# Kernel optimization log

Measured on AMD Instinct MI355X. Metric: run time of the kernel, lower is better.

The kernel has to match this reference:

```python
import jax, jax.numpy as jnp
import numpy as np

N = 8192      # grid points along the differentiated axis (axis=0)
B = 4096      # trailing batch/feature dim
S = 7         # stencil width (order=2, acc=4)


def _make_offsets(n, s):
    # Interior stencil is centered (-3..3); near boundaries the stencil is
    # shifted one-sided so that i + off stays in [0, n-1], matching the
    # precomputed one-sided boundary stencils of a non-uniform FD operator.
    i = np.arange(n)[:, None]                      # [n, 1]
    base = np.arange(s)[None, :] - s // 2          # [1, s]
    idx = np.clip(i + base, 0, n - 1)
    # de-duplicate clipped indices by re-spreading near boundaries
    lo_shift = np.maximum(0, (s // 2) - np.arange(n))[:, None]
    hi_shift = np.maximum(0, (s // 2) - (n - 1 - np.arange(n)))[:, None]
    idx = i + base + lo_shift - hi_shift           # valid, distinct indices
    return (idx - i).astype(np.int32)              # offsets relative to i


def setup_inputs() -> dict:
    key = jax.random.key(0)
    k1, k2 = jax.random.split(key)
    y = jax.random.normal(k1, (N, B), dtype=jnp.float32)
    all_coefficients = jax.random.normal(k2, (N, S), dtype=jnp.float32)
    all_offsets = jnp.asarray(_make_offsets(N, S))  # int32 [N, S]
    return {"y": y, "all_coefficients": all_coefficients, "all_offsets": all_offsets}


def reference(y, all_coefficients, all_offsets):
    # axis = 0, so y is already in 'moved' layout y_m.
    # Original: for each i, yd[i] = sum_s ws[i,s] * y[i + offs[i,s]]
    # (sequential fori_loop). Vectorized over all grid points i:
    n = y.shape[0]
    idxs = jnp.arange(n, dtype=all_offsets.dtype)[:, None] + all_offsets  # [n, S]
    stencil = jnp.take(y, idxs, axis=0)              # [n, S, B] gather
    yd = jnp.einsum('ns,ns...->n...', all_coefficients, stencil)
    return yd
```

## Files before the change

kernel.cpp:

```cpp
#include <hip/hip_runtime.h>


#define FD_N   8192
#define FD_B   4096
#define FD_S   7
#define FD_R   2
#define HALO   3
#define WIN    (FD_R + 2 * HALO)
#define NSTRIP (FD_N / FD_R)
#define NCHUNK 4
#define NWG    (NSTRIP * NCHUNK)
#define NXCD   8

typedef float v4f __attribute__((ext_vector_type(4)));

__global__ __launch_bounds__(256) void
_FinDiffNonUniform_51608327029442_kernel(const float* __restrict__ y,
                                         const float* __restrict__ coef,
                                         const int*   __restrict__ offs,
                                         float*       __restrict__ out) {
    const int bid   = blockIdx.x;
    const int id    = (bid & (NXCD - 1)) * (NWG / NXCD) + (bid >> 3);
    const int strip = id & (NSTRIP - 1);
    const int chunk = id >> 12;
    const int n0    = strip * FD_R;
    const int b     = (chunk << 10) + (threadIdx.x << 2);

    if (strip >= 2 && strip <= NSTRIP - 3) {
        float c[FD_R][FD_S];
#pragma unroll
        for (int r = 0; r < FD_R; ++r)
#pragma unroll
            for (int s = 0; s < FD_S; ++s)
                c[r][s] = coef[(size_t)(n0 + r) * FD_S + s];

        const float* ybase = y + (size_t)(n0 - HALO) * FD_B + b;

        v4f w[WIN];
#pragma unroll
        for (int j = 0; j < WIN; ++j)
            w[j] = *reinterpret_cast<const v4f*>(ybase + (size_t)j * FD_B);

        asm volatile("" ::: "memory");

        v4f acc[FD_R];
#pragma unroll
        for (int r = 0; r < FD_R; ++r)
            acc[r] = (v4f){0.f, 0.f, 0.f, 0.f};

#pragma unroll
        for (int j = 0; j < WIN; ++j) {
#pragma unroll
            for (int r = 0; r < FD_R; ++r) {
                const int s = j - r;
                if (s >= 0 && s < FD_S)
                    acc[r] += c[r][s] * w[j];
            }
        }

#pragma unroll
        for (int r = 0; r < FD_R; ++r)
            __builtin_nontemporal_store(
                acc[r], reinterpret_cast<v4f*>(out + (size_t)(n0 + r) * FD_B + b));
    } else {
#pragma unroll
        for (int r = 0; r < FD_R; ++r) {
            const int n = n0 + r;
            v4f acc = (v4f){0.f, 0.f, 0.f, 0.f};
#pragma unroll
            for (int s = 0; s < FD_S; ++s) {
                const float cc = coef[(size_t)n * FD_S + s];
                const int   o  = offs[(size_t)n * FD_S + s];
                const v4f   v  =
                    *reinterpret_cast<const v4f*>(y + (size_t)(n + o) * FD_B + b);
                acc += cc * v;
            }
            __builtin_nontemporal_store(
                acc, reinterpret_cast<v4f*>(out + (size_t)n * FD_B + b));
        }
    }
}

extern "C" void kernel_launch(void* const* d_in, const int* in_sizes, int n_in,
                              void* d_out, int out_size, void* d_ws, size_t ws_size,
                              hipStream_t stream) {
    const float* y    = (const float*)d_in[0];
    const float* coef = (const float*)d_in[1];
    const int*   offs = (const int*)d_in[2];
    float*       out  = (float*)d_out;

    _FinDiffNonUniform_51608327029442_kernel<<<NWG, 256, 0, stream>>>(y, coef, offs, out);
}
```

Measured before the change: 232.3 us.

## Stream a sliding register window over 32-row spans with prefetched rows

```diff
diff --git a/kernel.cpp b/kernel.cpp
--- a/kernel.cpp
+++ b/kernel.cpp
@@ -4,12 +4,14 @@
 #define FD_N   8192
 #define FD_B   4096
 #define FD_S   7
-#define FD_R   2
 #define HALO   3
-#define WIN    (FD_R + 2 * HALO)
-#define NSTRIP (FD_N / FD_R)
+#define STEP   4
+#define WIN    (STEP + 2 * HALO)
+#define SPAN   32
+#define NITER  (SPAN / STEP)
+#define NSPAN  (FD_N / SPAN)
 #define NCHUNK 4
-#define NWG    (NSTRIP * NCHUNK)
+#define NWG    (NSPAN * NCHUNK)
 #define NXCD   8
 
 typedef float v4f __attribute__((ext_vector_type(4)));
@@ -21,50 +23,14 @@
                                          float*       __restrict__ out) {
     const int bid   = blockIdx.x;
     const int id    = (bid & (NXCD - 1)) * (NWG / NXCD) + (bid >> 3);
-    const int strip = id & (NSTRIP - 1);
-    const int chunk = id >> 12;
-    const int n0    = strip * FD_R;
+    const int span  = id & (NSPAN - 1);
+    const int chunk = id >> 8;
+    const int n0    = span * SPAN;
     const int b     = (chunk << 10) + (threadIdx.x << 2);
 
-    if (strip >= 2 && strip <= NSTRIP - 3) {
-        float c[FD_R][FD_S];
-#pragma unroll
-        for (int r = 0; r < FD_R; ++r)
-#pragma unroll
-            for (int s = 0; s < FD_S; ++s)
-                c[r][s] = coef[(size_t)(n0 + r) * FD_S + s];
-
-        const float* ybase = y + (size_t)(n0 - HALO) * FD_B + b;
-
-        v4f w[WIN];
-#pragma unroll
-        for (int j = 0; j < WIN; ++j)
-            w[j] = *reinterpret_cast<const v4f*>(ybase + (size_t)j * FD_B);
-
-        asm volatile("" ::: "memory");
-
-        v4f acc[FD_R];
-#pragma unroll
-        for (int r = 0; r < FD_R; ++r)
-            acc[r] = (v4f){0.f, 0.f, 0.f, 0.f};
-
-#pragma unroll
-        for (int j = 0; j < WIN; ++j) {
-#pragma unroll
-            for (int r = 0; r < FD_R; ++r) {
-                const int s = j - r;
-                if (s >= 0 && s < FD_S)
-                    acc[r] += c[r][s] * w[j];
-            }
-        }
-
-#pragma unroll
-        for (int r = 0; r < FD_R; ++r)
-            __builtin_nontemporal_store(
-                acc[r], reinterpret_cast<v4f*>(out + (size_t)(n0 + r) * FD_B + b));
-    } else {
-#pragma unroll
-        for (int r = 0; r < FD_R; ++r) {
+    if (span == 0 || span == NSPAN - 1) {
+#pragma unroll 4
+        for (int r = 0; r < SPAN; ++r) {
             const int n = n0 + r;
             v4f acc = (v4f){0.f, 0.f, 0.f, 0.f};
 #pragma unroll
@@ -77,6 +43,54 @@
             }
             __builtin_nontemporal_store(
                 acc, reinterpret_cast<v4f*>(out + (size_t)n * FD_B + b));
+        }
+        return;
+    }
+
+    const float* ybase = y   + (size_t)(n0 - HALO) * FD_B + b;
+    float*       obase = out + (size_t)n0          * FD_B + b;
+
+    v4f w[WIN];
+#pragma unroll
+    for (int j = 0; j < WIN; ++j)
+        w[j] = *reinterpret_cast<const v4f*>(ybase + (size_t)j * FD_B);
+    asm volatile("" ::: "memory");
+
+#pragma unroll
+    for (int k = 0; k < NITER; ++k) {
+        const int a = k * STEP;
+
+        v4f p[STEP];
+        if (k + 1 < NITER) {
+#pragma unroll
+            for (int j = 0; j < STEP; ++j)
+                p[j] = *reinterpret_cast<const v4f*>(
+                           ybase + (size_t)(a + WIN + j) * FD_B);
+            asm volatile("" ::: "memory");
+        }
+
+        float c[STEP][FD_S];
+#pragma unroll
+        for (int r = 0; r < STEP; ++r)
+#pragma unroll
+            for (int s = 0; s < FD_S; ++s)
+                c[r][s] = coef[(size_t)(n0 + a + r) * FD_S + s];
+
+#pragma unroll
+        for (int r = 0; r < STEP; ++r) {
+            v4f acc = c[r][0] * w[r];
+#pragma unroll
+            for (int s = 1; s < FD_S; ++s)
+                acc += c[r][s] * w[r + s];
+            __builtin_nontemporal_store(
+                acc, reinterpret_cast<v4f*>(obase + (size_t)(a + r) * FD_B));
+        }
+
+        if (k + 1 < NITER) {
+#pragma unroll
+            for (int j = 0; j < WIN - STEP; ++j) w[j] = w[j + STEP];
+#pragma unroll
+            for (int j = 0; j < STEP; ++j)       w[WIN - STEP + j] = p[j];
         }
     }
 }
```

Measured after the change: 258.3 us. 11.2% more time.

## Stage stencil window in LDS via global_load_lds with larger row strips

Applied to the files above, without the earlier changes.

```diff
diff --git a/kernel.cpp b/kernel.cpp
--- a/kernel.cpp
+++ b/kernel.cpp
@@ -4,81 +4,96 @@
 #define FD_N   8192
 #define FD_B   4096
 #define FD_S   7
-#define FD_R   2
+#define FD_R   8
 #define HALO   3
 #define WIN    (FD_R + 2 * HALO)
 #define NSTRIP (FD_N / FD_R)
-#define NCHUNK 4
+#define CHUNKF 1024
+#define NCHUNK (FD_B / CHUNKF)
 #define NWG    (NSTRIP * NCHUNK)
-#define NXCD   8
 
 typedef float v4f __attribute__((ext_vector_type(4)));
+typedef unsigned int u32;
 
 __global__ __launch_bounds__(256) void
 _FinDiffNonUniform_51608327029442_kernel(const float* __restrict__ y,
                                          const float* __restrict__ coef,
                                          const int*   __restrict__ offs,
                                          float*       __restrict__ out) {
-    const int bid   = blockIdx.x;
-    const int id    = (bid & (NXCD - 1)) * (NWG / NXCD) + (bid >> 3);
-    const int strip = id & (NSTRIP - 1);
-    const int chunk = id >> 12;
+    const int strip = blockIdx.x >> 2;
+    const int chunk = blockIdx.x & 3;
     const int n0    = strip * FD_R;
-    const int b     = (chunk << 10) + (threadIdx.x << 2);
+    const int tid   = threadIdx.x;
+    const int b     = (chunk << 10) + (tid << 2);
 
-    if (strip >= 2 && strip <= NSTRIP - 3) {
-        float c[FD_R][FD_S];
-#pragma unroll
-        for (int r = 0; r < FD_R; ++r)
-#pragma unroll
-            for (int s = 0; s < FD_S; ++s)
-                c[r][s] = coef[(size_t)(n0 + r) * FD_S + s];
+    __shared__ float lds[WIN * CHUNKF];
 
-        const float* ybase = y + (size_t)(n0 - HALO) * FD_B + b;
-
-        v4f w[WIN];
-#pragma unroll
-        for (int j = 0; j < WIN; ++j)
-            w[j] = *reinterpret_cast<const v4f*>(ybase + (size_t)j * FD_B);
-
-        asm volatile("" ::: "memory");
-
-        v4f acc[FD_R];
-#pragma unroll
-        for (int r = 0; r < FD_R; ++r)
-            acc[r] = (v4f){0.f, 0.f, 0.f, 0.f};
-
-#pragma unroll
-        for (int j = 0; j < WIN; ++j) {
-#pragma unroll
-            for (int r = 0; r < FD_R; ++r) {
-                const int s = j - r;
-                if (s >= 0 && s < FD_S)
-                    acc[r] += c[r][s] * w[j];
-            }
-        }
-
-#pragma unroll
-        for (int r = 0; r < FD_R; ++r)
-            __builtin_nontemporal_store(
-                acc[r], reinterpret_cast<v4f*>(out + (size_t)(n0 + r) * FD_B + b));
-    } else {
+    if (strip == 0 || strip == NSTRIP - 1) {
 #pragma unroll
         for (int r = 0; r < FD_R; ++r) {
             const int n = n0 + r;
+            const float* __restrict__ c = coef + (size_t)n * FD_S;
+            const int*   __restrict__ o = offs + (size_t)n * FD_S;
             v4f acc = (v4f){0.f, 0.f, 0.f, 0.f};
 #pragma unroll
             for (int s = 0; s < FD_S; ++s) {
-                const float cc = coef[(size_t)n * FD_S + s];
-                const int   o  = offs[(size_t)n * FD_S + s];
-                const v4f   v  =
-                    *reinterpret_cast<const v4f*>(y + (size_t)(n + o) * FD_B + b);
-                acc += cc * v;
+                const v4f v = *reinterpret_cast<const v4f*>(
+                    y + (size_t)(n + o[s]) * FD_B + b);
+                acc += c[s] * v;
             }
             __builtin_nontemporal_store(
                 acc, reinterpret_cast<v4f*>(out + (size_t)n * FD_B + b));
         }
+        return;
     }
+
+    const int base = n0 - HALO;
+    const int wave = tid >> 6;
+    const int lane = tid & 63;
+
+    const char* gsrc = (const char*)y
+                     + (size_t)base * (FD_B * 4)
+                     + (size_t)chunk * (CHUNKF * 4)
+                     + (size_t)wave * 1024
+                     + (size_t)lane * 16;
+    u32* lbase = reinterpret_cast<u32*>(lds) + wave * 256;
+
+#pragma unroll
+    for (int j = 0; j < WIN; ++j) {
+        __builtin_amdgcn_global_load_lds(
+            (const __attribute__((address_space(1))) u32*)(gsrc + (size_t)j * (FD_B * 4)),
+            (__attribute__((address_space(3))) u32*)(lbase + j * CHUNKF),
+            16, 0, 0);
+    }
+    __syncthreads();
+
+    float c[FD_R][FD_S];
+#pragma unroll
+    for (int r = 0; r < FD_R; ++r)
+#pragma unroll
+        for (int s = 0; s < FD_S; ++s)
+            c[r][s] = coef[(size_t)(n0 + r) * FD_S + s];
+
+    v4f acc[FD_R];
+#pragma unroll
+    for (int r = 0; r < FD_R; ++r)
+        acc[r] = (v4f){0.f, 0.f, 0.f, 0.f};
+
+#pragma unroll
+    for (int j = 0; j < WIN; ++j) {
+        const v4f v = *reinterpret_cast<const v4f*>(&lds[j * CHUNKF + tid * 4]);
+#pragma unroll
+        for (int r = 0; r < FD_R; ++r) {
+            const int s = j - r;
+            if (s >= 0 && s < FD_S)
+                acc[r] += c[r][s] * v;
+        }
+    }
+
+#pragma unroll
+    for (int r = 0; r < FD_R; ++r)
+        __builtin_nontemporal_store(
+            acc[r], reinterpret_cast<v4f*>(out + (size_t)(n0 + r) * FD_B + b));
 }
 
 extern "C" void kernel_launch(void* const* d_in, const int* in_sizes, int n_in,
```

Measured after the change: 230.9 us. About the same (-0.6%).

## Stream rows through an LDS ring buffer with async global-to-LDS loads

Applied to the files above, without the earlier changes.

```diff
diff --git a/kernel.cpp b/kernel.cpp
--- a/kernel.cpp
+++ b/kernel.cpp
@@ -4,79 +4,117 @@
 #define FD_N   8192
 #define FD_B   4096
 #define FD_S   7
-#define FD_R   2
 #define HALO   3
-#define WIN    (FD_R + 2 * HALO)
-#define NSTRIP (FD_N / FD_R)
-#define NCHUNK 4
-#define NWG    (NSTRIP * NCHUNK)
-#define NXCD   8
+#define STEP   4
+#define NITER  16
+#define SPAN   (STEP * NITER)
+#define NBN    (FD_N / SPAN)
+#define NWG    (NBN * 4)
+#define RING   16
+#define SLOTF  256
+#define WIN    (STEP + 2 * HALO)
 
 typedef float v4f __attribute__((ext_vector_type(4)));
+typedef unsigned int u32;
+typedef const __attribute__((address_space(1))) u32* gptr_t;
+typedef __attribute__((address_space(3))) u32* lptr_t;
 
-__global__ __launch_bounds__(256) void
+__global__ __launch_bounds__(256, 2) void
 _FinDiffNonUniform_51608327029442_kernel(const float* __restrict__ y,
                                          const float* __restrict__ coef,
                                          const int*   __restrict__ offs,
                                          float*       __restrict__ out) {
-    const int bid   = blockIdx.x;
-    const int id    = (bid & (NXCD - 1)) * (NWG / NXCD) + (bid >> 3);
-    const int strip = id & (NSTRIP - 1);
-    const int chunk = id >> 12;
-    const int n0    = strip * FD_R;
-    const int b     = (chunk << 10) + (threadIdx.x << 2);
+    const int bn    = blockIdx.x >> 2;
+    const int chunk = blockIdx.x & 3;
+    const int n0    = bn * SPAN;
+    const int tid   = threadIdx.x;
+    const int wave  = tid >> 6;
+    const int lane  = tid & 63;
+    const int col   = (chunk << 10) + (wave << 8) + (lane << 2);
 
-    if (strip >= 2 && strip <= NSTRIP - 3) {
-        float c[FD_R][FD_S];
+    __shared__ float lds[4 * RING * SLOTF];
+    float* const wbase = lds + wave * (RING * SLOTF);
+
+    const bool lo = (bn == 0);
+    const bool hi = (bn == NBN - 1);
+
+    auto STAGE = [&](int r) {
+        int g = n0 - HALO + r;
+        g = g < 0 ? 0 : g;
+        g = g > FD_N - 1 ? FD_N - 1 : g;
+        const float* src = y + (size_t)g * FD_B + col;
+        __builtin_amdgcn_global_load_lds(
+            (gptr_t)src,
+            (lptr_t)((u32*)wbase + (r & (RING - 1)) * SLOTF),
+            16, 0, 0);
+    };
+
 #pragma unroll
-        for (int r = 0; r < FD_R; ++r)
+    for (int r = 0; r < 12; ++r) STAGE(r);
+
 #pragma unroll
-            for (int s = 0; s < FD_S; ++s)
-                c[r][s] = coef[(size_t)(n0 + r) * FD_S + s];
-
-        const float* ybase = y + (size_t)(n0 - HALO) * FD_B + b;
+    for (int k = 0; k < NITER; ++k) {
+        if (k == 0) asm volatile("s_waitcnt vmcnt(2)" ::: "memory");
+        else        asm volatile("s_waitcnt vmcnt(6)" ::: "memory");
 
         v4f w[WIN];
 #pragma unroll
-        for (int j = 0; j < WIN; ++j)
-            w[j] = *reinterpret_cast<const v4f*>(ybase + (size_t)j * FD_B);
+        for (int m = 0; m < WIN; ++m)
+            w[m] = *reinterpret_cast<const v4f*>(
+                wbase + ((4 * k + m) & (RING - 1)) * SLOTF + (lane << 2));
 
         asm volatile("" ::: "memory");
 
-        v4f acc[FD_R];
+        if (k < NITER - 1) {
+            STAGE(4 * k + 12);
+            STAGE(4 * k + 13);
+            STAGE(4 * k + 14);
+            STAGE(4 * k + 15);
+        }
+
+        float c[STEP][FD_S];
 #pragma unroll
-        for (int r = 0; r < FD_R; ++r)
-            acc[r] = (v4f){0.f, 0.f, 0.f, 0.f};
+        for (int j = 0; j < STEP; ++j)
+#pragma unroll
+            for (int s = 0; s < FD_S; ++s)
+                c[j][s] = coef[(size_t)(n0 + 4 * k + j) * FD_S + s];
+
+        v4f acc[STEP];
+#pragma unroll
+        for (int j = 0; j < STEP; ++j) acc[j] = (v4f){0.f, 0.f, 0.f, 0.f};
 
 #pragma unroll
-        for (int j = 0; j < WIN; ++j) {
+        for (int m = 0; m < WIN; ++m)
 #pragma unroll
-            for (int r = 0; r < FD_R; ++r) {
-                const int s = j - r;
+            for (int j = 0; j < STEP; ++j) {
+                const int s = m - j;
                 if (s >= 0 && s < FD_S)
-                    acc[r] += c[r][s] * w[j];
+                    acc[j] += c[j][s] * w[m];
             }
-        }
 
 #pragma unroll
-        for (int r = 0; r < FD_R; ++r)
+        for (int j = 0; j < STEP; ++j)
             __builtin_nontemporal_store(
-                acc[r], reinterpret_cast<v4f*>(out + (size_t)(n0 + r) * FD_B + b));
-    } else {
+                acc[j],
+                reinterpret_cast<v4f*>(out + (size_t)(n0 + 4 * k + j) * FD_B + col));
+    }
+
+    if (lo || hi) {
+        asm volatile("s_waitcnt vmcnt(0)" ::: "memory");
+        const int nbeg = lo ? 0 : FD_N - HALO;
 #pragma unroll
-        for (int r = 0; r < FD_R; ++r) {
-            const int n = n0 + r;
+        for (int t = 0; t < HALO; ++t) {
+            const int n = nbeg + t;
+            const float* __restrict__ cc = coef + (size_t)n * FD_S;
+            const int*   __restrict__ oo = offs + (size_t)n * FD_S;
             v4f acc = (v4f){0.f, 0.f, 0.f, 0.f};
 #pragma unroll
             for (int s = 0; s < FD_S; ++s) {
-                const float cc = coef[(size_t)n * FD_S + s];
-                const int   o  = offs[(size_t)n * FD_S + s];
-                const v4f   v  =
-                    *reinterpret_cast<const v4f*>(y + (size_t)(n + o) * FD_B + b);
-                acc += cc * v;
+                const v4f v = *reinterpret_cast<const v4f*>(
+                    y + (size_t)(n + oo[s]) * FD_B + col);
+                acc += cc[s] * v;
             }
-            __builtin_nontemporal_store(
-                acc, reinterpret_cast<v4f*>(out + (size_t)n * FD_B + b));
+            *reinterpret_cast<v4f*>(out + (size_t)n * FD_B + col) = acc;
         }
     }
 }
```

Result: no change. 233.3 us (+0.4%).
